# Kernel optimization log

Measured on AMD Instinct MI355X. Metric: run time of the kernel, lower is better.

## Reference

```python
import jax, jax.numpy as jnp
import numpy as np

B, S, D, H, DH = 4, 2048, 1024, 16, 64


def setup_inputs() -> dict:
    key = jax.random.key(0)
    ks = jax.random.split(key, 12)
    inp = {
        "query": jax.random.normal(ks[0], (B, S, D), jnp.float32),
        "key": jax.random.normal(ks[1], (B, S, D), jnp.float32),
        "value": jax.random.normal(ks[2], (B, S, D), jnp.float32),
        # causal mask, broadcast over batch and heads
        "mask": jnp.tril(jnp.ones((S, S), jnp.int32))[None, None, :, :],
        "Wq": jax.random.normal(ks[3], (D, D), jnp.float32) * 0.02,
        "bq": jnp.zeros((D,), jnp.float32),
        "Wk": jax.random.normal(ks[4], (D, D), jnp.float32) * 0.02,
        "bk": jnp.zeros((D,), jnp.float32),
        "Wv": jax.random.normal(ks[5], (D, D), jnp.float32) * 0.02,
        "bv": jnp.zeros((D,), jnp.float32),
        "Wo": jax.random.normal(ks[6], (D, D), jnp.float32) * 0.02,
        "bo": jnp.zeros((D,), jnp.float32),
    }
    return inp


def reference(query, key, value, mask, Wq, bq, Wk, bk, Wv, bv, Wo, bo):
    # linear projections (torch Linear: x @ W^T + b; here W stored as [in, out])
    q = query @ Wq + bq
    k = key @ Wk + bk
    v = value @ Wv + bv
    # [B, S, D] -> [B, H, S, DH]
    q = q.reshape(B, S, H, DH).transpose(0, 2, 1, 3)
    k = k.reshape(B, S, H, DH).transpose(0, 2, 1, 3)
    v = v.reshape(B, S, H, DH).transpose(0, 2, 1, 3)
    # materialized O(S^2) attention scores
    scores = jnp.einsum("bhqd,bhkd->bhqk", q, k) * (DH ** -0.5)
    scores = jnp.where(mask == 0, jnp.float32(-jnp.inf), scores)
    attn = jax.nn.softmax(scores, axis=-1)  # dropout is identity in eval
    x = jnp.einsum("bhqk,bhkd->bhqd", attn, v)
    # [B, H, S, DH] -> [B, S, D]
    x = x.transpose(0, 2, 1, 3).reshape(B, S, D)
    out = x @ Wo + bo
    return out
```

## Files before the change

kernel.cpp:

```cpp
#include <hip/hip_runtime.h>
#include <hip/hip_bf16.h>


typedef __bf16 bf16x8 __attribute__((ext_vector_type(8)));
typedef float f32x4 __attribute__((ext_vector_type(4)));

#define GLOBAL_AS __attribute__((address_space(1)))
#define LDS_AS __attribute__((address_space(3)))

static __device__ __forceinline__ unsigned short f2bf(float f) {
    __bf16 h = (__bf16)f;
    return __builtin_bit_cast(unsigned short, h);
}

static __device__ __forceinline__ void gload_lds16(const void* g, void* l) {
    __builtin_amdgcn_global_load_lds((const GLOBAL_AS void*)g, (LDS_AS void*)l, 16, 0, 0);
}

__global__ __launch_bounds__(256) void cvt_f32_bf16(const float* __restrict__ src,
                                                    unsigned short* __restrict__ dst, int n8) {
    int i = blockIdx.x * 256 + threadIdx.x;
    if (i >= n8) return;
    const float4* s = (const float4*)src + 2 * (size_t)i;
    float4 v0 = s[0], v1 = s[1];
    unsigned short h[8] = {f2bf(v0.x), f2bf(v0.y), f2bf(v0.z), f2bf(v0.w),
                           f2bf(v1.x), f2bf(v1.y), f2bf(v1.z), f2bf(v1.w)};
    *(uint4*)(dst + 8 * (size_t)i) = *(const uint4*)h;
}

__global__ void transpose_weights(const float* __restrict__ W0, const float* __restrict__ W1,
                                  const float* __restrict__ W2, const float* __restrict__ W3,
                                  unsigned short* __restrict__ T0, unsigned short* __restrict__ T1,
                                  unsigned short* __restrict__ T2, unsigned short* __restrict__ T3) {
    const float* W; unsigned short* T;
    switch (blockIdx.z) { case 0: W=W0; T=T0; break; case 1: W=W1; T=T1; break;
                          case 2: W=W2; T=T2; break; default: W=W3; T=T3; }
    __shared__ float tile[32][33];
    int tx = threadIdx.x, ty = threadIdx.y;
    int k0 = blockIdx.x * 32, n0 = blockIdx.y * 32;
#pragma unroll
    for (int j = 0; j < 4; j++) tile[ty + 8*j][tx] = W[(size_t)(k0 + ty + 8*j) * 1024 + n0 + tx];
    __syncthreads();
#pragma unroll
    for (int j = 0; j < 4; j++) T[(size_t)(n0 + ty + 8*j) * 1024 + k0 + tx] = f2bf(tile[tx][ty + 8*j]);
}

template <int MODE>
__global__ __launch_bounds__(256) void gemm_bt(const unsigned short* __restrict__ A,
                                               const unsigned short* __restrict__ BT,
                                               const float* __restrict__ bias,
                                               void* __restrict__ Out) {
    __shared__ unsigned short Asm[128 * 64];
    __shared__ unsigned short Bsm[128 * 64];
    const int t = threadIdx.x;
    const int lane = t & 63, w = t >> 6;
    const int g = lane >> 4, r16 = lane & 15;
    const int wr = w >> 1, wc = w & 1;
    const int rowBase = blockIdx.y * 128, colBase = blockIdx.x * 128;
    const int K = 1024;
    const int srow = t >> 3;
    const int scol = (t & 7) * 8;

    const unsigned short* srcA[4];
    const unsigned short* srcB[4];
#pragma unroll
    for (int j = 0; j < 4; j++) {
        srcA[j] = A  + (size_t)(rowBase + srow + 32 * j) * K + scol;
        srcB[j] = BT + (size_t)(colBase + srow + 32 * j) * K + scol;
    }
    unsigned short* dstA = Asm + 512 * w;
    unsigned short* dstB = Bsm + 512 * w;

    f32x4 acc[4][4] = {};

    for (int k0 = 0; k0 < K; k0 += 64) {
        __syncthreads();
#pragma unroll
        for (int j = 0; j < 4; j++) {
            gload_lds16(srcA[j] + k0, dstA + 2048 * j);
            gload_lds16(srcB[j] + k0, dstB + 2048 * j);
        }
        __syncthreads();
#pragma unroll
        for (int ks = 0; ks < 2; ks++) {
            bf16x8 a[4], b[4];
#pragma unroll
            for (int m = 0; m < 4; m++) {
                int row = 64 * wr + 16 * m + r16;
                a[m] = *(const bf16x8*)(Asm + row * 64 + 32 * ks + 8 * g);
            }
#pragma unroll
            for (int n = 0; n < 4; n++) {
                int row = 64 * wc + 16 * n + r16;
                b[n] = *(const bf16x8*)(Bsm + row * 64 + 32 * ks + 8 * g);
            }
#pragma unroll
            for (int m = 0; m < 4; m++)
#pragma unroll
                for (int n = 0; n < 4; n++)
                    acc[m][n] = __builtin_amdgcn_mfma_f32_16x16x32_bf16(a[m], b[n], acc[m][n], 0, 0, 0);
        }
    }

    float bv[4];
#pragma unroll
    for (int n = 0; n < 4; n++) bv[n] = bias[colBase + 64 * wc + 16 * n + r16];

#pragma unroll
    for (int m = 0; m < 4; m++) {
#pragma unroll
        for (int n = 0; n < 4; n++) {
#pragma unroll
            for (int i = 0; i < 4; i++) {
                int row = rowBase + 64 * wr + 16 * m + 4 * g + i;
                int col = colBase + 64 * wc + 16 * n + r16;
                float v = acc[m][n][i] + bv[n];
                if constexpr (MODE == 3) {
                    ((float*)Out)[(size_t)row * 1024 + col] = v;
                } else {
                    int bidx = row >> 11, s = row & 2047;
                    int hidx = col >> 6, dh = col & 63;
                    if constexpr (MODE == 0) v *= 0.125f;
                    if constexpr (MODE == 2)
                        ((unsigned short*)Out)[(((size_t)(bidx * 16 + hidx)) * 64 + dh) * 2048 + s] = f2bf(v);
                    else
                        ((unsigned short*)Out)[(((size_t)(bidx * 16 + hidx)) * 2048 + s) * 64 + dh] = f2bf(v);
                }
            }
        }
    }
}

__global__ __launch_bounds__(256) void attn_kernel(const unsigned short* __restrict__ Q,
                                                   const unsigned short* __restrict__ Kb,
                                                   const unsigned short* __restrict__ VT,
                                                   unsigned short* __restrict__ Xout) {
    __shared__ unsigned short Ksm[2][64 * 64];
    __shared__ unsigned short Vsm[2][64 * 64];
    const int t = threadIdx.x;
    const int lane = t & 63, w = t >> 6;
    const int g = lane >> 4, q16 = lane & 15;
    const int bh = blockIdx.y;
    const int b = bh >> 4, h = bh & 15;

    const int srow0 = t >> 3;
    const int ssrc = ((t & 7) ^ (srow0 & 7)) * 8;
    const unsigned short* srcK[2];
    const unsigned short* srcV[2];
#pragma unroll
    for (int j = 0; j < 2; j++) {
        int row = srow0 + 32 * j;
        srcK[j] = Kb + ((size_t)bh * 2048 + row) * 64 + ssrc;
        srcV[j] = VT + ((size_t)bh * 64 + row) * 2048 + ssrc;
    }

    const int gh = g >> 1;
    const int g0 = 2 * (g & 1);
    const int srcA = 16 * g0 + q16, srcB = srcA + 16;

#pragma unroll 1
    for (int ph = 0; ph < 2; ph++) {
        const int qt = ph ? (31 - (int)blockIdx.x) : (int)blockIdx.x;
        const int q0 = qt * 64;
        const int myq = q0 + 16 * w + q16;
        const int nkt = qt + 1;

        bf16x8 qfrag[2];
        {
            const uint4* qp = (const uint4*)(Q + ((size_t)bh * 2048 + myq) * 64);
            qfrag[0] = __builtin_bit_cast(bf16x8, qp[g]);
            qfrag[1] = __builtin_bit_cast(bf16x8, qp[4 + g]);
        }

        f32x4 acco[4] = {};
        float m = -1e30f, lsum = 0.f;
        int cur = 0;

#pragma unroll
        for (int j = 0; j < 2; j++) {
            gload_lds16(srcK[j], &Ksm[0][512 * w + 2048 * j]);
            gload_lds16(srcV[j], &Vsm[0][512 * w + 2048 * j]);
        }
        __syncthreads();

        for (int kt = 0; kt < nkt; kt++) {
            const int k0 = kt * 64;
            if (kt + 1 < nkt) {
                int nxt = cur ^ 1;
#pragma unroll
                for (int j = 0; j < 2; j++) {
                    gload_lds16(srcK[j] + (size_t)(kt + 1) * 4096, &Ksm[nxt][512 * w + 2048 * j]);
                    gload_lds16(srcV[j] + (size_t)(kt + 1) * 64,   &Vsm[nxt][512 * w + 2048 * j]);
                }
            }

            f32x4 accS[4] = {};
#pragma unroll
            for (int ks = 0; ks < 2; ks++) {
#pragma unroll
                for (int tt = 0; tt < 4; tt++) {
                    int row = 16 * tt + q16;
                    bf16x8 ak = *(const bf16x8*)(&Ksm[cur][row * 64 + ((4 * ks + g) ^ (row & 7)) * 8]);
                    accS[tt] = __builtin_amdgcn_mfma_f32_16x16x32_bf16(ak, qfrag[ks], accS[tt], 0, 0, 0);
                }
            }

            const bool lastTile = (kt == nkt - 1);
            float s[4][4];
#pragma unroll
            for (int tt = 0; tt < 4; tt++)
#pragma unroll
                for (int i = 0; i < 4; i++) {
                    float v = accS[tt][i];
                    if (lastTile) {
                        int kg = k0 + 16 * tt + 4 * g + i;
                        if (kg > myq) v = -1e30f;
                    }
                    s[tt][i] = v;
                }

            float pmax = -1e30f;
#pragma unroll
            for (int tt = 0; tt < 4; tt++)
#pragma unroll
                for (int i = 0; i < 4; i++) pmax = fmaxf(pmax, s[tt][i]);
            pmax = fmaxf(pmax, __shfl_xor(pmax, 16));
            pmax = fmaxf(pmax, __shfl_xor(pmax, 32));

            float mnew = fmaxf(m, pmax);
            float sc = __expf(m - mnew);
            m = mnew;

            float tsum = 0.f;
            float p[4][4];
#pragma unroll
            for (int tt = 0; tt < 4; tt++)
#pragma unroll
                for (int i = 0; i < 4; i++) { p[tt][i] = __expf(s[tt][i] - mnew); tsum += p[tt][i]; }
            tsum += __shfl_xor(tsum, 16);
            tsum += __shfl_xor(tsum, 32);
            lsum = lsum * sc + tsum;

            unsigned lo[4], hi[4];
#pragma unroll
            for (int tt = 0; tt < 4; tt++) {
                lo[tt] = (unsigned)f2bf(p[tt][0]) | ((unsigned)f2bf(p[tt][1]) << 16);
                hi[tt] = (unsigned)f2bf(p[tt][2]) | ((unsigned)f2bf(p[tt][3]) << 16);
            }

#pragma unroll
            for (int i = 0; i < 4; i++) {
                float sci = __shfl(sc, 4 * g + i);
#pragma unroll
                for (int d = 0; d < 4; d++) acco[d][i] *= sci;
            }

#pragma unroll
            for (int ks = 0; ks < 2; ks++) {
                unsigned xa0 = __shfl(lo[2 * ks], srcA);
                unsigned xa1 = __shfl(hi[2 * ks], srcA);
                unsigned xa2 = __shfl(lo[2 * ks], srcB);
                unsigned xa3 = __shfl(hi[2 * ks], srcB);
                unsigned ya0 = __shfl(lo[2 * ks + 1], srcA);
                unsigned ya1 = __shfl(hi[2 * ks + 1], srcA);
                unsigned ya2 = __shfl(lo[2 * ks + 1], srcB);
                unsigned ya3 = __shfl(hi[2 * ks + 1], srcB);
                uint4 pw;
                pw.x = gh ? ya0 : xa0;
                pw.y = gh ? ya1 : xa1;
                pw.z = gh ? ya2 : xa2;
                pw.w = gh ? ya3 : xa3;
                bf16x8 pfrag = __builtin_bit_cast(bf16x8, pw);
#pragma unroll
                for (int d = 0; d < 4; d++) {
                    int row = 16 * d + q16;
                    bf16x8 vv = *(const bf16x8*)(&Vsm[cur][row * 64 + ((4 * ks + g) ^ (row & 7)) * 8]);
                    acco[d] = __builtin_amdgcn_mfma_f32_16x16x32_bf16(pfrag, vv, acco[d], 0, 0, 0);
                }
            }

            __syncthreads();
            cur ^= 1;
        }

#pragma unroll
        for (int i = 0; i < 4; i++) {
            float li = __shfl(lsum, 4 * g + i);
            float inv = 1.f / li;
            int row = q0 + 16 * w + 4 * g + i;
#pragma unroll
            for (int d = 0; d < 4; d++) {
                int col = h * 64 + 16 * d + q16;
                Xout[((size_t)b * 2048 + row) * 1024 + col] = f2bf(acco[d][i] * inv);
            }
        }
        __syncthreads();
    }
}

extern "C" void kernel_launch(void* const* d_in, const int* in_sizes, int n_in,
                              void* d_out, int out_size, void* d_ws, size_t ws_size,
                              hipStream_t stream) {
    (void)in_sizes; (void)n_in; (void)out_size; (void)ws_size;
    const float* query = (const float*)d_in[0];
    const float* key   = (const float*)d_in[1];
    const float* value = (const float*)d_in[2];
    const float* Wq = (const float*)d_in[4];
    const float* bq = (const float*)d_in[5];
    const float* Wk = (const float*)d_in[6];
    const float* bk = (const float*)d_in[7];
    const float* Wv = (const float*)d_in[8];
    const float* bv = (const float*)d_in[9];
    const float* Wo = (const float*)d_in[10];
    const float* bo = (const float*)d_in[11];

    char* base = (char*)d_ws;
    const size_t MB = 1u << 20;
    unsigned short* WTq = (unsigned short*)(base + 0 * MB);
    unsigned short* WTk = (unsigned short*)(base + 2 * MB);
    unsigned short* WTv = (unsigned short*)(base + 4 * MB);
    unsigned short* WTo = (unsigned short*)(base + 6 * MB);
    unsigned short* Qb  = (unsigned short*)(base + 8 * MB);
    unsigned short* Kbf = (unsigned short*)(base + 24 * MB);
    unsigned short* VTb = (unsigned short*)(base + 40 * MB);
    unsigned short* X   = (unsigned short*)(base + 56 * MB);

    const int n8 = (8192 * 1024) / 8;

    transpose_weights<<<dim3(32, 32, 4), dim3(32, 8), 0, stream>>>(Wq, Wk, Wv, Wo, WTq, WTk, WTv, WTo);

    cvt_f32_bf16<<<4096, 256, 0, stream>>>(query, X, n8);
    gemm_bt<0><<<dim3(8, 64), 256, 0, stream>>>(X, WTq, bq, Qb);
    cvt_f32_bf16<<<4096, 256, 0, stream>>>(key, X, n8);
    gemm_bt<1><<<dim3(8, 64), 256, 0, stream>>>(X, WTk, bk, Kbf);
    cvt_f32_bf16<<<4096, 256, 0, stream>>>(value, X, n8);
    gemm_bt<2><<<dim3(8, 64), 256, 0, stream>>>(X, WTv, bv, VTb);

    attn_kernel<<<dim3(16, 64), 256, 0, stream>>>(Qb, Kbf, VTb, X);
    gemm_bt<3><<<dim3(8, 64), 256, 0, stream>>>(X, WTo, bo, (float*)d_out);
}
```

Before: 385.2 us.

## Batch QKV projections and interleave paired query tiles in attention

Merges the three input conversions and the three QKV projection GEMMs into single launches indexed by blockIdx.z, using the output buffer as scratch for the key and value bf16 copies. The attention kernel now processes both query tiles of a causal pair in one pass over the K/V tiles, so each loaded K/V tile serves both. It also folds log2(e) into the Q scale so softmax can use exp2, skips the rescale of the running max when the new max grows by less than 8, and raises wave priority around the MFMA sections. Register pressure rises from keeping two accumulator sets live, and the lazy rescale adds some numerical risk.

```diff
diff --git a/kernel.cpp b/kernel.cpp
--- a/kernel.cpp
+++ b/kernel.cpp
@@ -7,6 +7,13 @@
 
 #define GLOBAL_AS __attribute__((address_space(1)))
 #define LDS_AS __attribute__((address_space(3)))
+
+#if __has_builtin(__builtin_amdgcn_exp2f)
+#define EXP2(x) __builtin_amdgcn_exp2f(x)
+#else
+#define EXP2(x) __expf((x) * 0.6931471805599453f)
+#endif
+#define QSCALE 0.18033688f
 
 static __device__ __forceinline__ unsigned short f2bf(float f) {
     __bf16 h = (__bf16)f;
@@ -17,8 +24,15 @@
     __builtin_amdgcn_global_load_lds((const GLOBAL_AS void*)g, (LDS_AS void*)l, 16, 0, 0);
 }
 
-__global__ __launch_bounds__(256) void cvt_f32_bf16(const float* __restrict__ src,
-                                                    unsigned short* __restrict__ dst, int n8) {
+__global__ __launch_bounds__(256) void cvt3(const float* __restrict__ q,
+                                            const float* __restrict__ k,
+                                            const float* __restrict__ v,
+                                            unsigned short* __restrict__ dq,
+                                            unsigned short* __restrict__ dk,
+                                            unsigned short* __restrict__ dv, int n8) {
+    const int z = blockIdx.z;
+    const float* src = (z == 0) ? q : (z == 1) ? k : v;
+    unsigned short* dst = (z == 0) ? dq : (z == 1) ? dk : dv;
     int i = blockIdx.x * 256 + threadIdx.x;
     if (i >= n8) return;
     const float4* s = (const float4*)src + 2 * (size_t)i;
@@ -45,66 +59,84 @@
     for (int j = 0; j < 4; j++) T[(size_t)(n0 + ty + 8*j) * 1024 + k0 + tx] = f2bf(tile[tx][ty + 8*j]);
 }
 
-template <int MODE>
-__global__ __launch_bounds__(256) void gemm_bt(const unsigned short* __restrict__ A,
-                                               const unsigned short* __restrict__ BT,
-                                               const float* __restrict__ bias,
-                                               void* __restrict__ Out) {
-    __shared__ unsigned short Asm[128 * 64];
-    __shared__ unsigned short Bsm[128 * 64];
+static __device__ __forceinline__ void gemm_core(const unsigned short* __restrict__ A,
+                                                 const unsigned short* __restrict__ BT,
+                                                 unsigned short* Asm, unsigned short* Bsm,
+                                                 int rowBase, int colBase, int t,
+                                                 f32x4 acc[4][4]) {
+    const int lane = t & 63, w = t >> 6;
+    const int g = lane >> 4, r16 = lane & 15;
+    const int wr = w >> 1, wc = w & 1;
+    const int K = 1024;
+    const int srow = t >> 3;
+    const int scol = (t & 7) * 8;
+
+    const unsigned short* srcA[4];
+    const unsigned short* srcB[4];
+#pragma unroll
+    for (int j = 0; j < 4; j++) {
+        srcA[j] = A  + (size_t)(rowBase + srow + 32 * j) * K + scol;
+        srcB[j] = BT + (size_t)(colBase + srow + 32 * j) * K + scol;
+    }
+    unsigned short* dstA = Asm + 512 * w;
+    unsigned short* dstB = Bsm + 512 * w;
+
+    for (int k0 = 0; k0 < K; k0 += 64) {
+        __syncthreads();
+#pragma unroll
+        for (int j = 0; j < 4; j++) {
+            gload_lds16(srcA[j] + k0, dstA + 2048 * j);
+            gload_lds16(srcB[j] + k0, dstB + 2048 * j);
+        }
+        __syncthreads();
+#pragma unroll
+        for (int ks = 0; ks < 2; ks++) {
+            bf16x8 a[4], b[4];
+#pragma unroll
+            for (int m = 0; m < 4; m++) {
+                int row = 64 * wr + 16 * m + r16;
+                a[m] = *(const bf16x8*)(Asm + row * 64 + 32 * ks + 8 * g);
+            }
+#pragma unroll
+            for (int n = 0; n < 4; n++) {
+                int row = 64 * wc + 16 * n + r16;
+                b[n] = *(const bf16x8*)(Bsm + row * 64 + 32 * ks + 8 * g);
+            }
+#pragma unroll
+            for (int m = 0; m < 4; m++)
+#pragma unroll
+                for (int n = 0; n < 4; n++)
+                    acc[m][n] = __builtin_amdgcn_mfma_f32_16x16x32_bf16(a[m], b[n], acc[m][n], 0, 0, 0);
+        }
+    }
+}
+
+__global__ __launch_bounds__(256) void gemm_qkv(
+        const unsigned short* __restrict__ Xq, const unsigned short* __restrict__ Xk,
+        const unsigned short* __restrict__ Xv,
+        const unsigned short* __restrict__ WTq, const unsigned short* __restrict__ WTk,
+        const unsigned short* __restrict__ WTv,
+        const float* __restrict__ bq, const float* __restrict__ bk, const float* __restrict__ bv,
+        unsigned short* __restrict__ Qb, unsigned short* __restrict__ Kb,
+        unsigned short* __restrict__ VT) {
+    __shared__ alignas(16) unsigned short Asm[8192];
+    __shared__ alignas(16) unsigned short Bsm[8192];
+    const int z = blockIdx.z;
+    const unsigned short* A  = (z == 0) ? Xq : (z == 1) ? Xk : Xv;
+    const unsigned short* BT = (z == 0) ? WTq : (z == 1) ? WTk : WTv;
+    const float* bias        = (z == 0) ? bq : (z == 1) ? bk : bv;
+    const int rowBase = blockIdx.y * 128, colBase = blockIdx.x * 128;
     const int t = threadIdx.x;
     const int lane = t & 63, w = t >> 6;
     const int g = lane >> 4, r16 = lane & 15;
     const int wr = w >> 1, wc = w & 1;
-    const int rowBase = blockIdx.y * 128, colBase = blockIdx.x * 128;
-    const int K = 1024;
-    const int srow = t >> 3;
-    const int scol = (t & 7) * 8;
-
-    const unsigned short* srcA[4];
-    const unsigned short* srcB[4];
-#pragma unroll
-    for (int j = 0; j < 4; j++) {
-        srcA[j] = A  + (size_t)(rowBase + srow + 32 * j) * K + scol;
-        srcB[j] = BT + (size_t)(colBase + srow + 32 * j) * K + scol;
-    }
-    unsigned short* dstA = Asm + 512 * w;
-    unsigned short* dstB = Bsm + 512 * w;
 
     f32x4 acc[4][4] = {};
-
-    for (int k0 = 0; k0 < K; k0 += 64) {
-        __syncthreads();
-#pragma unroll
-        for (int j = 0; j < 4; j++) {
-            gload_lds16(srcA[j] + k0, dstA + 2048 * j);
-            gload_lds16(srcB[j] + k0, dstB + 2048 * j);
-        }
-        __syncthreads();
-#pragma unroll
-        for (int ks = 0; ks < 2; ks++) {
-            bf16x8 a[4], b[4];
-#pragma unroll
-            for (int m = 0; m < 4; m++) {
-                int row = 64 * wr + 16 * m + r16;
-                a[m] = *(const bf16x8*)(Asm + row * 64 + 32 * ks + 8 * g);
-            }
-#pragma unroll
-            for (int n = 0; n < 4; n++) {
-                int row = 64 * wc + 16 * n + r16;
-                b[n] = *(const bf16x8*)(Bsm + row * 64 + 32 * ks + 8 * g);
-            }
-#pragma unroll
-            for (int m = 0; m < 4; m++)
-#pragma unroll
-                for (int n = 0; n < 4; n++)
-                    acc[m][n] = __builtin_amdgcn_mfma_f32_16x16x32_bf16(a[m], b[n], acc[m][n], 0, 0, 0);
-        }
-    }
-
-    float bv[4];
-#pragma unroll
-    for (int n = 0; n < 4; n++) bv[n] = bias[colBase + 64 * wc + 16 * n + r16];
+    gemm_core(A, BT, Asm, Bsm, rowBase, colBase, t, acc);
+
+    float bv4[4];
+#pragma unroll
+    for (int n = 0; n < 4; n++) bv4[n] = bias[colBase + 64 * wc + 16 * n + r16];
 
 #pragma unroll
     for (int m = 0; m < 4; m++) {
@@ -114,20 +146,142 @@
             for (int i = 0; i < 4; i++) {
                 int row = rowBase + 64 * wr + 16 * m + 4 * g + i;
                 int col = colBase + 64 * wc + 16 * n + r16;
-                float v = acc[m][n][i] + bv[n];
-                if constexpr (MODE == 3) {
-                    ((float*)Out)[(size_t)row * 1024 + col] = v;
-                } else {
-                    int bidx = row >> 11, s = row & 2047;
-                    int hidx = col >> 6, dh = col & 63;
-                    if constexpr (MODE == 0) v *= 0.125f;
-                    if constexpr (MODE == 2)
-                        ((unsigned short*)Out)[(((size_t)(bidx * 16 + hidx)) * 64 + dh) * 2048 + s] = f2bf(v);
-                    else
-                        ((unsigned short*)Out)[(((size_t)(bidx * 16 + hidx)) * 2048 + s) * 64 + dh] = f2bf(v);
-                }
-            }
-        }
+                float v = acc[m][n][i] + bv4[n];
+                int bidx = row >> 11, s = row & 2047;
+                int hidx = col >> 6, dh = col & 63;
+                size_t bh = (size_t)(bidx * 16 + hidx);
+                if (z == 0)      Qb[(bh * 2048 + s) * 64 + dh] = f2bf(v * QSCALE);
+                else if (z == 1) Kb[(bh * 2048 + s) * 64 + dh] = f2bf(v);
+                else             VT[(bh * 64 + dh) * 2048 + s] = f2bf(v);
+            }
+        }
+    }
+}
+
+__global__ __launch_bounds__(256) void gemm_out(const unsigned short* __restrict__ A,
+                                                const unsigned short* __restrict__ BT,
+                                                const float* __restrict__ bias,
+                                                float* __restrict__ Out) {
+    __shared__ alignas(16) unsigned short Asm[8192];
+    __shared__ alignas(16) unsigned short Bsm[8192];
+    const int rowBase = blockIdx.y * 128, colBase = blockIdx.x * 128;
+    const int t = threadIdx.x;
+    const int lane = t & 63, w = t >> 6;
+    const int g = lane >> 4, r16 = lane & 15;
+    const int wr = w >> 1, wc = w & 1;
+
+    f32x4 acc[4][4] = {};
+    gemm_core(A, BT, Asm, Bsm, rowBase, colBase, t, acc);
+
+    float bv4[4];
+#pragma unroll
+    for (int n = 0; n < 4; n++) bv4[n] = bias[colBase + 64 * wc + 16 * n + r16];
+
+#pragma unroll
+    for (int m = 0; m < 4; m++)
+#pragma unroll
+        for (int n = 0; n < 4; n++)
+#pragma unroll
+            for (int i = 0; i < 4; i++) {
+                int row = rowBase + 64 * wr + 16 * m + 4 * g + i;
+                int col = colBase + 64 * wc + 16 * n + r16;
+                Out[(size_t)row * 1024 + col] = acc[m][n][i] + bv4[n];
+            }
+}
+
+static __device__ __forceinline__ void attn_step(
+        const unsigned short* __restrict__ Ks, const unsigned short* __restrict__ Vs,
+        const bf16x8 qfrag[2], f32x4 acco[4], float& m, float& lsum,
+        int myq, int k0, bool diag,
+        int g, int q16, int gh, int srcA, int srcB) {
+    f32x4 accS[4] = {};
+    __builtin_amdgcn_s_setprio(1);
+#pragma unroll
+    for (int ks = 0; ks < 2; ks++) {
+#pragma unroll
+        for (int tt = 0; tt < 4; tt++) {
+            int row = 16 * tt + q16;
+            bf16x8 ak = *(const bf16x8*)(Ks + row * 64 + ((4 * ks + g) ^ (row & 7)) * 8);
+            accS[tt] = __builtin_amdgcn_mfma_f32_16x16x32_bf16(ak, qfrag[ks], accS[tt], 0, 0, 0);
+        }
+    }
+    __builtin_amdgcn_s_setprio(0);
+
+    float s[4][4];
+#pragma unroll
+    for (int tt = 0; tt < 4; tt++)
+#pragma unroll
+        for (int i = 0; i < 4; i++) {
+            float v = accS[tt][i];
+            if (diag) {
+                int kg = k0 + 16 * tt + 4 * g + i;
+                if (kg > myq) v = -1e30f;
+            }
+            s[tt][i] = v;
+        }
+
+    float pmax = s[0][0];
+#pragma unroll
+    for (int tt = 0; tt < 4; tt++)
+#pragma unroll
+        for (int i = 0; i < 4; i++) pmax = fmaxf(pmax, s[tt][i]);
+    pmax = fmaxf(pmax, __shfl_xor(pmax, 16));
+    pmax = fmaxf(pmax, __shfl_xor(pmax, 32));
+
+    if (!__all(pmax <= m + 8.0f)) {
+        float mnew = fmaxf(m, pmax);
+        float sc = EXP2(m - mnew);
+        lsum *= sc;
+#pragma unroll
+        for (int i = 0; i < 4; i++) {
+            float sci = __shfl(sc, 4 * g + i);
+#pragma unroll
+            for (int d = 0; d < 4; d++) acco[d][i] *= sci;
+        }
+        m = mnew;
+    }
+
+    float tsum = 0.f;
+    float p[4][4];
+#pragma unroll
+    for (int tt = 0; tt < 4; tt++)
+#pragma unroll
+        for (int i = 0; i < 4; i++) { p[tt][i] = EXP2(s[tt][i] - m); tsum += p[tt][i]; }
+    tsum += __shfl_xor(tsum, 16);
+    tsum += __shfl_xor(tsum, 32);
+    lsum += tsum;
+
+    unsigned lo[4], hi[4];
+#pragma unroll
+    for (int tt = 0; tt < 4; tt++) {
+        lo[tt] = (unsigned)f2bf(p[tt][0]) | ((unsigned)f2bf(p[tt][1]) << 16);
+        hi[tt] = (unsigned)f2bf(p[tt][2]) | ((unsigned)f2bf(p[tt][3]) << 16);
+    }
+
+#pragma unroll
+    for (int ks = 0; ks < 2; ks++) {
+        unsigned xa0 = __shfl(lo[2 * ks], srcA);
+        unsigned xa1 = __shfl(hi[2 * ks], srcA);
+        unsigned xa2 = __shfl(lo[2 * ks], srcB);
+        unsigned xa3 = __shfl(hi[2 * ks], srcB);
+        unsigned ya0 = __shfl(lo[2 * ks + 1], srcA);
+        unsigned ya1 = __shfl(hi[2 * ks + 1], srcA);
+        unsigned ya2 = __shfl(lo[2 * ks + 1], srcB);
+        unsigned ya3 = __shfl(hi[2 * ks + 1], srcB);
+        uint4 pw;
+        pw.x = gh ? ya0 : xa0;
+        pw.y = gh ? ya1 : xa1;
+        pw.z = gh ? ya2 : xa2;
+        pw.w = gh ? ya3 : xa3;
+        bf16x8 pfrag = __builtin_bit_cast(bf16x8, pw);
+        __builtin_amdgcn_s_setprio(1);
+#pragma unroll
+        for (int d = 0; d < 4; d++) {
+            int row = 16 * d + q16;
+            bf16x8 vv = *(const bf16x8*)(Vs + row * 64 + ((4 * ks + g) ^ (row & 7)) * 8);
+            acco[d] = __builtin_amdgcn_mfma_f32_16x16x32_bf16(pfrag, vv, acco[d], 0, 0, 0);
+        }
+        __builtin_amdgcn_s_setprio(0);
     }
 }
 
@@ -135,13 +289,17 @@
                                                    const unsigned short* __restrict__ Kb,
                                                    const unsigned short* __restrict__ VT,
                                                    unsigned short* __restrict__ Xout) {
-    __shared__ unsigned short Ksm[2][64 * 64];
-    __shared__ unsigned short Vsm[2][64 * 64];
+    __shared__ alignas(16) unsigned short Ksm[2][4096];
+    __shared__ alignas(16) unsigned short Vsm[2][4096];
     const int t = threadIdx.x;
     const int lane = t & 63, w = t >> 6;
     const int g = lane >> 4, q16 = lane & 15;
     const int bh = blockIdx.y;
     const int b = bh >> 4, h = bh & 15;
+    const int bx = blockIdx.x;
+    const int qtA = bx, qtB = 31 - bx;
+    const int myqA = qtA * 64 + 16 * w + q16;
+    const int myqB = qtB * 64 + 16 * w + q16;
 
     const int srow0 = t >> 3;
     const int ssrc = ((t & 7) ^ (srow0 & 7)) * 8;
@@ -158,143 +316,61 @@
     const int g0 = 2 * (g & 1);
     const int srcA = 16 * g0 + q16, srcB = srcA + 16;
 
+    bf16x8 qfA[2], qfB[2];
+    {
+        const uint4* qp = (const uint4*)(Q + ((size_t)bh * 2048 + myqA) * 64);
+        qfA[0] = __builtin_bit_cast(bf16x8, qp[g]);
+        qfA[1] = __builtin_bit_cast(bf16x8, qp[4 + g]);
+        const uint4* qq = (const uint4*)(Q + ((size_t)bh * 2048 + myqB) * 64);
+        qfB[0] = __builtin_bit_cast(bf16x8, qq[g]);
+        qfB[1] = __builtin_bit_cast(bf16x8, qq[4 + g]);
+    }
+
+    f32x4 accoA[4] = {}, accoB[4] = {};
+    float mA = -1e30f, lsA = 0.f, mB = -1e30f, lsB = 0.f;
+    int cur = 0;
+
+#pragma unroll
+    for (int j = 0; j < 2; j++) {
+        gload_lds16(srcK[j], &Ksm[0][512 * w + 2048 * j]);
+        gload_lds16(srcV[j], &Vsm[0][512 * w + 2048 * j]);
+    }
+    __syncthreads();
+
+    const int nkt = qtB + 1;
 #pragma unroll 1
-    for (int ph = 0; ph < 2; ph++) {
-        const int qt = ph ? (31 - (int)blockIdx.x) : (int)blockIdx.x;
-        const int q0 = qt * 64;
-        const int myq = q0 + 16 * w + q16;
-        const int nkt = qt + 1;
-
-        bf16x8 qfrag[2];
-        {
-            const uint4* qp = (const uint4*)(Q + ((size_t)bh * 2048 + myq) * 64);
-            qfrag[0] = __builtin_bit_cast(bf16x8, qp[g]);
-            qfrag[1] = __builtin_bit_cast(bf16x8, qp[4 + g]);
-        }
-
-        f32x4 acco[4] = {};
-        float m = -1e30f, lsum = 0.f;
-        int cur = 0;
-
-#pragma unroll
-        for (int j = 0; j < 2; j++) {
-            gload_lds16(srcK[j], &Ksm[0][512 * w + 2048 * j]);
-            gload_lds16(srcV[j], &Vsm[0][512 * w + 2048 * j]);
-        }
+    for (int kt = 0; kt < nkt; kt++) {
+        if (kt + 1 < nkt) {
+            int nxt = cur ^ 1;
+#pragma unroll
+            for (int j = 0; j < 2; j++) {
+                gload_lds16(srcK[j] + (size_t)(kt + 1) * 4096, &Ksm[nxt][512 * w + 2048 * j]);
+                gload_lds16(srcV[j] + (size_t)(kt + 1) * 64,   &Vsm[nxt][512 * w + 2048 * j]);
+            }
+        }
+        const unsigned short* Ks = Ksm[cur];
+        const unsigned short* Vs = Vsm[cur];
+        attn_step(Ks, Vs, qfB, accoB, mB, lsB, myqB, kt * 64, kt == qtB, g, q16, gh, srcA, srcB);
+        if (kt <= qtA)
+            attn_step(Ks, Vs, qfA, accoA, mA, lsA, myqA, kt * 64, kt == qtA, g, q16, gh, srcA, srcB);
         __syncthreads();
-
-        for (int kt = 0; kt < nkt; kt++) {
-            const int k0 = kt * 64;
-            if (kt + 1 < nkt) {
-                int nxt = cur ^ 1;
-#pragma unroll
-                for (int j = 0; j < 2; j++) {
-                    gload_lds16(srcK[j] + (size_t)(kt + 1) * 4096, &Ksm[nxt][512 * w + 2048 * j]);
-                    gload_lds16(srcV[j] + (size_t)(kt + 1) * 64,   &Vsm[nxt][512 * w + 2048 * j]);
-                }
-            }
-
-            f32x4 accS[4] = {};
-#pragma unroll
-            for (int ks = 0; ks < 2; ks++) {
-#pragma unroll
-                for (int tt = 0; tt < 4; tt++) {
-                    int row = 16 * tt + q16;
-                    bf16x8 ak = *(const bf16x8*)(&Ksm[cur][row * 64 + ((4 * ks + g) ^ (row & 7)) * 8]);
-                    accS[tt] = __builtin_amdgcn_mfma_f32_16x16x32_bf16(ak, qfrag[ks], accS[tt], 0, 0, 0);
-                }
-            }
-
-            const bool lastTile = (kt == nkt - 1);
-            float s[4][4];
-#pragma unroll
-            for (int tt = 0; tt < 4; tt++)
-#pragma unroll
-                for (int i = 0; i < 4; i++) {
-                    float v = accS[tt][i];
-                    if (lastTile) {
-                        int kg = k0 + 16 * tt + 4 * g + i;
-                        if (kg > myq) v = -1e30f;
-                    }
-                    s[tt][i] = v;
-                }
-
-            float pmax = -1e30f;
-#pragma unroll
-            for (int tt = 0; tt < 4; tt++)
-#pragma unroll
-                for (int i = 0; i < 4; i++) pmax = fmaxf(pmax, s[tt][i]);
-            pmax = fmaxf(pmax, __shfl_xor(pmax, 16));
-            pmax = fmaxf(pmax, __shfl_xor(pmax, 32));
-
-            float mnew = fmaxf(m, pmax);
-            float sc = __expf(m - mnew);
-            m = mnew;
-
-            float tsum = 0.f;
-            float p[4][4];
-#pragma unroll
-            for (int tt = 0; tt < 4; tt++)
-#pragma unroll
-                for (int i = 0; i < 4; i++) { p[tt][i] = __expf(s[tt][i] - mnew); tsum += p[tt][i]; }
-            tsum += __shfl_xor(tsum, 16);
-            tsum += __shfl_xor(tsum, 32);
-            lsum = lsum * sc + tsum;
-
-            unsigned lo[4], hi[4];
-#pragma unroll
-            for (int tt = 0; tt < 4; tt++) {
-                lo[tt] = (unsigned)f2bf(p[tt][0]) | ((unsigned)f2bf(p[tt][1]) << 16);
-                hi[tt] = (unsigned)f2bf(p[tt][2]) | ((unsigned)f2bf(p[tt][3]) << 16);
-            }
-
-#pragma unroll
-            for (int i = 0; i < 4; i++) {
-                float sci = __shfl(sc, 4 * g + i);
-#pragma unroll
-                for (int d = 0; d < 4; d++) acco[d][i] *= sci;
-            }
-
-#pragma unroll
-            for (int ks = 0; ks < 2; ks++) {
-                unsigned xa0 = __shfl(lo[2 * ks], srcA);
-                unsigned xa1 = __shfl(hi[2 * ks], srcA);
-                unsigned xa2 = __shfl(lo[2 * ks], srcB);
-                unsigned xa3 = __shfl(hi[2 * ks], srcB);
-                unsigned ya0 = __shfl(lo[2 * ks + 1], srcA);
-                unsigned ya1 = __shfl(hi[2 * ks + 1], srcA);
-                unsigned ya2 = __shfl(lo[2 * ks + 1], srcB);
-                unsigned ya3 = __shfl(hi[2 * ks + 1], srcB);
-                uint4 pw;
-                pw.x = gh ? ya0 : xa0;
-                pw.y = gh ? ya1 : xa1;
-                pw.z = gh ? ya2 : xa2;
-                pw.w = gh ? ya3 : xa3;
-                bf16x8 pfrag = __builtin_bit_cast(bf16x8, pw);
-#pragma unroll
-                for (int d = 0; d < 4; d++) {
-                    int row = 16 * d + q16;
-                    bf16x8 vv = *(const bf16x8*)(&Vsm[cur][row * 64 + ((4 * ks + g) ^ (row & 7)) * 8]);
-                    acco[d] = __builtin_amdgcn_mfma_f32_16x16x32_bf16(pfrag, vv, acco[d], 0, 0, 0);
-                }
-            }
-
-            __syncthreads();
-            cur ^= 1;
-        }
-
-#pragma unroll
-        for (int i = 0; i < 4; i++) {
-            float li = __shfl(lsum, 4 * g + i);
-            float inv = 1.f / li;
-            int row = q0 + 16 * w + 4 * g + i;
-#pragma unroll
-            for (int d = 0; d < 4; d++) {
-                int col = h * 64 + 16 * d + q16;
-                Xout[((size_t)b * 2048 + row) * 1024 + col] = f2bf(acco[d][i] * inv);
-            }
-        }
-        __syncthreads();
+        cur ^= 1;
+    }
+
+#pragma unroll
+    for (int i = 0; i < 4; i++) {
+        float liB = __shfl(lsB, 4 * g + i);
+        float invB = 1.f / liB;
+        int rowB = qtB * 64 + 16 * w + 4 * g + i;
+        float liA = __shfl(lsA, 4 * g + i);
+        float invA = 1.f / liA;
+        int rowA = qtA * 64 + 16 * w + 4 * g + i;
+#pragma unroll
+        for (int d = 0; d < 4; d++) {
+            int col = h * 64 + 16 * d + q16;
+            Xout[((size_t)b * 2048 + rowB) * 1024 + col] = f2bf(accoB[d][i] * invB);
+            Xout[((size_t)b * 2048 + rowA) * 1024 + col] = f2bf(accoA[d][i] * invA);
+        }
     }
 }
 
@@ -325,17 +401,14 @@
     unsigned short* VTb = (unsigned short*)(base + 40 * MB);
     unsigned short* X   = (unsigned short*)(base + 56 * MB);
 
+    unsigned short* Xk = (unsigned short*)d_out;
+    unsigned short* Xv = Xk + (size_t)8192 * 1024;
+
     const int n8 = (8192 * 1024) / 8;
 
     transpose_weights<<<dim3(32, 32, 4), dim3(32, 8), 0, stream>>>(Wq, Wk, Wv, Wo, WTq, WTk, WTv, WTo);
-
-    cvt_f32_bf16<<<4096, 256, 0, stream>>>(query, X, n8);
-    gemm_bt<0><<<dim3(8, 64), 256, 0, stream>>>(X, WTq, bq, Qb);
-    cvt_f32_bf16<<<4096, 256, 0, stream>>>(key, X, n8);
-    gemm_bt<1><<<dim3(8, 64), 256, 0, stream>>>(X, WTk, bk, Kbf);
-    cvt_f32_bf16<<<4096, 256, 0, stream>>>(value, X, n8);
-    gemm_bt<2><<<dim3(8, 64), 256, 0, stream>>>(X, WTv, bv, VTb);
-
+    cvt3<<<dim3(4096, 1, 3), 256, 0, stream>>>(query, key, value, X, Xk, Xv, n8);
+    gemm_qkv<<<dim3(8, 64, 3), 256, 0, stream>>>(X, Xk, Xv, WTq, WTk, WTv, bq, bk, bv, Qb, Kbf, VTb);
     attn_kernel<<<dim3(16, 64), 256, 0, stream>>>(Qb, Kbf, VTb, X);
-    gemm_bt<3><<<dim3(8, 64), 256, 0, stream>>>(X, WTo, bo, (float*)d_out);
-}
+    gemm_out<<<dim3(8, 64), 256, 0, stream>>>(X, WTo, bo, (float*)d_out);
+}
```

Result: slower. 408.7 us (+6.1%).
